# Optimization experiments

Measured on AMD Instinct MI355X. Metric: run time of the kernel, lower is better.

Reference implementation:

```python
import jax, jax.numpy as jnp
import numpy as np

N, E, W, H, NXF, NDF = 131072, 8, 128, 64, 10, 4
DX = 3 + 3 * 2 * NXF  # 63
DV = 3 + 3 * 2 * NDF  # 27
TEMP = 0.166667


def pe(x, degree):
    # positional encoding: [x, sin(2^i x), cos(2^i x)]
    y = jnp.concatenate([(2.0 ** i) * x for i in range(degree)], -1)
    return jnp.concatenate([x, jnp.sin(y), jnp.cos(y)], -1)


def setup_inputs() -> dict:
    key = jax.random.key(0)
    ks = jax.random.split(key, 8)
    s = 0.05
    return {
        'x': jax.random.normal(ks[0], (N, 6), jnp.float32),
        'W_enc': jax.random.normal(ks[1], (DX, W), jnp.float32) * s,
        'b_enc': jnp.zeros((W,), jnp.float32),
        'W_sh': jax.random.normal(ks[2], (E, W, W), jnp.float32) * s,
        'b_sh': jnp.zeros((E, W), jnp.float32),
        'w_sig': jax.random.normal(ks[3], (W,), jnp.float32) * s,
        'b_sig': jnp.zeros((1,), jnp.float32),
        'W_r1': jax.random.normal(ks[4], (E, W + DV, H), jnp.float32) * s,
        'b_r1': jnp.zeros((E, H), jnp.float32),
        'W_r2': jax.random.normal(ks[5], (E, H, 3), jnp.float32) * s,
        'b_r2': jnp.zeros((E, 3), jnp.float32),
    }


def reference(x, W_enc, b_enc, W_sh, b_sh, w_sig, b_sig, W_r1, b_r1, W_r2, b_r2):
    xyz = pe(x[:, :3], NXF)          # [N, 63]
    vd = pe(x[:, 3:6], NDF)          # [N, 27]
    y = jax.nn.relu(xyz @ W_enc + b_enc)  # encoding_xyz -> [N, W]
    # all shape experts at once: [N, E, W]
    shape_out = jax.nn.relu(jnp.einsum('nd,edh->neh', y, W_sh) + b_sh)
    # shared sigma head, softplus keeps sigma > 0: [N, E]
    sigmas = jax.nn.softplus(jnp.einsum('neh,h->ne', shape_out, w_sig) + b_sig)
    log_logits = jax.nn.log_softmax(jnp.log(sigmas + 1e-10) / TEMP, axis=-1)
    # gumbel-softmax (tau=1, torch default) with fixed noise key
    u = jax.random.uniform(jax.random.key(42), sigmas.shape, jnp.float32)
    g = -jnp.log(-jnp.log(u + 1e-20) + 1e-20)
    gates_soft = jax.nn.softmax(log_logits + g, axis=-1)
    index = jnp.argmax(gates_soft, axis=-1)  # [N]
    hard = jax.nn.one_hot(index, E, dtype=sigmas.dtype)
    # straight-through hard gates
    gates_hard = hard - jax.lax.stop_gradient(gates_soft) + gates_soft
    sigmas_pooled = jnp.take_along_axis(sigmas, index[:, None], axis=-1)  # [N, 1]
    # rgb experts: concat(shape_out_i, viewdir) -> MLP -> sigmoid rgb, gated sum
    vdb = jnp.broadcast_to(vd[:, None, :], (vd.shape[0], E, DV))
    inp = jnp.concatenate([shape_out, vdb], axis=-1)  # [N, E, W+27]
    h = jax.nn.relu(jnp.einsum('nec,ech->neh', inp, W_r1) + b_r1)
    rgb = jax.nn.sigmoid(jnp.einsum('neh,eho->neo', h, W_r2) + b_r2)  # [N, E, 3]
    rgbs = jnp.sum(rgb * gates_hard[:, :, None], axis=1)  # [N, 3]
    return jnp.concatenate([rgbs, sigmas_pooled], axis=-1)  # [N, 4]
```

## Files before the change

### kernel.cpp

```cpp
#include <hip/hip_runtime.h>
#include <hip/hip_bf16.h>


#define NPTS 131072
#define PT 64
#define NTH 256
#define NBLK (NPTS / PT)
#define INV2048 (1.0f / 2048.0f)

#define WS_ENC_H 0
#define WS_ENC_L 8192
#define WS_SH_H  16384
#define WS_SH_L  147456
#define WS_R1_H  278528

#define OFF_YH   0
#define OFF_B    17408
#define OFF_RED  38912
#define SMEM_SZ  40960

#define S_LIST(s) (*(int*)(smem + OFF_B + (s) * 336 + 320))
#define S_BID(p)  (*(int*)(smem + OFF_B + (p) * 336 + 324))
#define S_CNT(e)  (*(int*)(smem + OFF_B + (e) * 336 + 328))
#define S_OFF(e)  (*(int*)(smem + OFF_B + (e) * 336 + 332))

typedef __attribute__((ext_vector_type(8))) _Float16 f16x8;
typedef __attribute__((ext_vector_type(4))) _Float16 f16x4;
typedef __attribute__((ext_vector_type(4))) float f32x4;

#define MFMA(a, b, c) __builtin_amdgcn_mfma_f32_16x16x32_f16((a), (b), (c), 0, 0, 0)

__device__ __forceinline__ unsigned rotl32(unsigned x, int d) {
  return (x << d) | (x >> (32 - d));
}

__device__ __forceinline__ float gumbel_for(unsigned flat) {
  const unsigned k0 = 0u, k1 = 42u;
  const unsigned ks2 = k0 ^ k1 ^ 0x1BD11BDAu;
  unsigned x0 = 0u + k0;
  unsigned x1 = flat + k1;
#define TF_RND(r) { x0 += x1; x1 = rotl32(x1, r); x1 ^= x0; }
  TF_RND(13) TF_RND(15) TF_RND(26) TF_RND(6)
  x0 += k1;  x1 += ks2 + 1u;
  TF_RND(17) TF_RND(29) TF_RND(16) TF_RND(24)
  x0 += ks2; x1 += k0 + 2u;
  TF_RND(13) TF_RND(15) TF_RND(26) TF_RND(6)
  x0 += k0;  x1 += k1 + 3u;
  TF_RND(17) TF_RND(29) TF_RND(16) TF_RND(24)
  x0 += k1;  x1 += ks2 + 4u;
  TF_RND(13) TF_RND(15) TF_RND(26) TF_RND(6)
  x0 += ks2; x1 += k0 + 5u;
#undef TF_RND
  unsigned bits = x0 ^ x1;
  float u = __uint_as_float((bits >> 9) | 0x3f800000u) - 1.0f;
  return -logf(-logf(u + 1e-20f) + 1e-20f);
}

__global__ void prep_kernel(const float* __restrict__ W_enc,
                            const float* __restrict__ W_sh,
                            const float* __restrict__ W_r1,
                            _Float16* __restrict__ ws) {
  int idx = blockIdx.x * 256 + threadIdx.x;
  if (idx < 8192) {
    int tile = idx >> 9, r = idx & 511;
    int L = r >> 3, j = r & 7;
    int nt = tile >> 1, kt = tile & 1;
    int k = kt * 32 + (L >> 4) * 8 + j;
    int n = nt * 16 + (L & 15);
    float v = (k < 63) ? W_enc[k * 128 + n] : 0.0f;
    _Float16 h = (_Float16)v;
    ws[WS_ENC_H + idx] = h;
    ws[WS_ENC_L + idx] = (_Float16)((v - (float)h) * 2048.0f);
  } else if (idx < 8192 + 131072) {
    int s = idx - 8192;
    int tile = s >> 9, r = s & 511;
    int L = r >> 3, j = r & 7;
    int e = tile >> 5, nt = (tile >> 2) & 7, kt = tile & 3;
    int k = kt * 32 + (L >> 4) * 8 + j;
    int n = nt * 16 + (L & 15);
    float v = W_sh[e * 16384 + k * 128 + n];
    _Float16 h = (_Float16)v;
    ws[WS_SH_H + s] = h;
    ws[WS_SH_L + s] = (_Float16)((v - (float)h) * 2048.0f);
  } else if (idx < 8192 + 131072 + 81920) {
    int s = idx - (8192 + 131072);
    int tile = s >> 9, r = s & 511;
    int L = r >> 3, j = r & 7;
    int e = tile / 20, rr = tile % 20;
    int nt = rr / 5, kt = rr % 5;
    int k = kt * 32 + (L >> 4) * 8 + j;
    int n = nt * 16 + (L & 15);
    float v = (k < 155) ? W_r1[e * 9920 + k * 64 + n] : 0.0f;
    ws[WS_R1_H + s] = (_Float16)v;
  }
}

__global__ __launch_bounds__(NTH, 3)
void nerf_moe_kernel(const float* __restrict__ x,
                     const float* __restrict__ b_enc,
                     const float* __restrict__ b_sh,
                     const float* __restrict__ w_sig, const float* __restrict__ b_sig,
                     const float* __restrict__ b_r1,
                     const float* __restrict__ W_r2,  const float* __restrict__ b_r2,
                     const _Float16* __restrict__ wsw,
                     float* __restrict__ out) {
  __shared__ __align__(16) unsigned char smem[SMEM_SZ];
  _Float16* sYh  = (_Float16*)(smem + OFF_YH);
  float*    sH   = (float*)(smem + OFF_YH);
  _Float16* sYl  = (_Float16*)(smem + OFF_B);
  _Float16* sPEh = (_Float16*)(smem + OFF_B);
  _Float16* sPEl = (_Float16*)(smem + OFF_B + 9216);
  _Float16* sSB  = (_Float16*)(smem + OFF_B);
  float*    sRed = (float*)(smem + OFF_RED);

  const int t  = threadIdx.x;
  const int w  = t >> 6;
  const int L  = t & 63;
  const int q  = L >> 4;
  const int c  = L & 15;
  const int n0 = blockIdx.x * PT;

  sRed[t] = 0.0f;
  sRed[t + 256] = 0.0f;

  for (int idx = t; idx < PT * 64; idx += NTH) {
    int p = idx >> 6, f = idx & 63;
    const float* xr = x + (size_t)(n0 + p) * 6;
    float v;
    if (f < 3)       v = xr[f];
    else if (f < 33) { int g = f - 3;  v = sinf(xr[g % 3] * (float)(1 << (g / 3))); }
    else if (f < 63) { int g = f - 33; v = cosf(xr[g % 3] * (float)(1 << (g / 3))); }
    else             v = 0.0f;
    _Float16 h = (_Float16)v;
    sPEh[p * 72 + f] = h;
    sPEl[p * 72 + f] = (_Float16)((v - (float)h) * 2048.0f);
  }
  __syncthreads();

  {
    f16x8 beh[2][2], bel[2][2];
    #pragma unroll
    for (int ntL = 0; ntL < 2; ++ntL)
      #pragma unroll
      for (int kt = 0; kt < 2; ++kt) {
        int tile = (2 * w + ntL) * 2 + kt;
        beh[ntL][kt] = *(const f16x8*)(wsw + WS_ENC_H + tile * 512 + L * 8);
        bel[ntL][kt] = *(const f16x8*)(wsw + WS_ENC_L + tile * 512 + L * 8);
      }
    f32x4 a1[4][2], a2[4][2];
    #pragma unroll
    for (int mt = 0; mt < 4; ++mt)
      #pragma unroll
      for (int ntL = 0; ntL < 2; ++ntL) { a1[mt][ntL] = (f32x4)0.0f; a2[mt][ntL] = (f32x4)0.0f; }
    #pragma unroll
    for (int half = 0; half < 2; ++half) {
      f16x8 pah[2][2], pal[2][2];
      #pragma unroll
      for (int m = 0; m < 2; ++m)
        #pragma unroll
        for (int kt = 0; kt < 2; ++kt) {
          int off = ((half * 2 + m) * 16 + c) * 72 + kt * 32 + q * 8;
          pah[m][kt] = *(const f16x8*)(sPEh + off);
          pal[m][kt] = *(const f16x8*)(sPEl + off);
        }
      #pragma unroll
      for (int kt = 0; kt < 2; ++kt)
        #pragma unroll
        for (int m = 0; m < 2; ++m)
          #pragma unroll
          for (int ntL = 0; ntL < 2; ++ntL) {
            int mt = half * 2 + m;
            a1[mt][ntL] = MFMA(pah[m][kt], beh[ntL][kt], a1[mt][ntL]);
            a2[mt][ntL] = MFMA(pah[m][kt], bel[ntL][kt], a2[mt][ntL]);
            a2[mt][ntL] = MFMA(pal[m][kt], beh[ntL][kt], a2[mt][ntL]);
          }
      asm volatile("" ::: "memory");
    }
    __syncthreads();
    float bb0 = b_enc[(2 * w) * 16 + c];
    float bb1 = b_enc[(2 * w + 1) * 16 + c];
    #pragma unroll
    for (int mt = 0; mt < 4; ++mt)
      #pragma unroll
      for (int ntL = 0; ntL < 2; ++ntL) {
        float bb = ntL ? bb1 : bb0;
        int col = (2 * w + ntL) * 16 + c;
        #pragma unroll
        for (int r = 0; r < 4; ++r) {
          float v = fmaxf(a1[mt][ntL][r] + a2[mt][ntL][r] * INV2048 + bb, 0.0f);
          int row = mt * 16 + q * 4 + r;
          _Float16 h = (_Float16)v;
          sYh[row * 136 + col] = h;
          sYl[row * 136 + col] = (_Float16)((v - (float)h) * 2048.0f);
        }
      }
  }
  __syncthreads();

  f16x8 Ah[4][3];
  #pragma unroll
  for (int nt = 0; nt < 4; ++nt)
    #pragma unroll
    for (int kt = 0; kt < 3; ++kt)
      Ah[nt][kt] = *(const f16x8*)(sYh + (nt * 16 + c) * 136 + kt * 32 + q * 8);
  const f32x4 wsv0 = *(const f32x4*)(w_sig + (2 * w) * 16 + q * 4);
  const f32x4 wsv1 = *(const f32x4*)(w_sig + (2 * w + 1) * 16 + q * 4);

  float psum[4] = {0.f, 0.f, 0.f, 0.f};

  #pragma unroll 1
  for (int s = 0; s < 16; ++s) {
    int e = s >> 1, i = s & 1;
    int tbase = (e * 8 + 2 * w + i) * 4;
    f16x8 bh[4], bl[4];
    #pragma unroll
    for (int kt = 0; kt < 4; ++kt) {
      bh[kt] = *(const f16x8*)(wsw + WS_SH_H + (tbase + kt) * 512 + L * 8);
      bl[kt] = *(const f16x8*)(wsw + WS_SH_L + (tbase + kt) * 512 + L * 8);
    }
    f32x4 bb = *(const f32x4*)(b_sh + e * 128 + (2 * w + i) * 16 + q * 4);

    f32x4 a1[4], a2[4];
    #pragma unroll
    for (int nt = 0; nt < 4; ++nt) { a1[nt] = (f32x4)0.0f; a2[nt] = (f32x4)0.0f; }
    #pragma unroll
    for (int kt = 0; kt < 4; ++kt)
      #pragma unroll
      for (int nt = 0; nt < 4; ++nt) {
        f16x8 al = *(const f16x8*)(sYl + (nt * 16 + c) * 136 + kt * 32 + q * 8);
        f16x8 ah;
        if (kt < 3) ah = Ah[nt][kt];
        else        ah = *(const f16x8*)(sYh + (nt * 16 + c) * 136 + kt * 32 + q * 8);
        a1[nt] = MFMA(bh[kt], ah, a1[nt]);
        a2[nt] = MFMA(bl[kt], ah, a2[nt]);
        a2[nt] = MFMA(bh[kt], al, a2[nt]);
      }
    f32x4 wv = (s & 1) ? wsv1 : wsv0;
    #pragma unroll
    for (int nt = 0; nt < 4; ++nt)
      #pragma unroll
      for (int r = 0; r < 4; ++r) {
        float sv = fmaxf(fmaf(a2[nt][r], INV2048, a1[nt][r]) + bb[r], 0.0f);
        psum[nt] = fmaf(sv, wv[r], psum[nt]);
      }
    if (s & 1) {
      #pragma unroll
      for (int nt = 0; nt < 4; ++nt) {
        float v = psum[nt];
        v += __shfl_xor(v, 16);
        v += __shfl_xor(v, 32);
        if (q == 0) atomicAdd(sRed + e * 64 + nt * 16 + c, v);
        psum[nt] = 0.f;
      }
    }
  }
  __syncthreads();

  {
    int pt = t >> 2;
    int eb = (t & 3) * 2;
    float best = -1e30f, bsig = 0.0f;
    int bide = 0;
    const float bs = b_sig[0];
    #pragma unroll
    for (int j = 0; j < 2; ++j) {
      int e = eb + j;
      float s = sRed[e * 64 + pt];
      float dotv = s + bs;
      float sig = fmaxf(dotv, 0.0f) + log1pf(expf(-fabsf(dotv)));
      float z = logf(sig + 1e-10f) / 0.166667f;
      float score = z + gumbel_for((unsigned)((n0 + pt) * 8 + e));
      if (score > best) { best = score; bsig = sig; bide = e; }
    }
    #pragma unroll
    for (int m = 1; m <= 2; m <<= 1) {
      float oS  = __shfl_xor(best, m);
      float oSg = __shfl_xor(bsig, m);
      int   oI  = __shfl_xor(bide, m);
      if (oS > best || (oS == best && oI < bide)) { best = oS; bsig = oSg; bide = oI; }
    }
    if ((t & 3) == 0) {
      S_BID(pt) = bide;
      out[(size_t)(n0 + pt) * 4 + 3] = bsig;
    }
  }
  __syncthreads();

  if (t < 8) {
    int cnt = 0;
    for (int p = 0; p < PT; ++p) cnt += (S_BID(p) == t);
    S_CNT(t) = cnt;
  }
  __syncthreads();
  if (t < 8) {
    int off = 0;
    for (int i = 0; i < t; ++i) off += S_CNT(i);
    S_OFF(t) = off;
    int k = off;
    for (int p = 0; p < PT; ++p) if (S_BID(p) == t) { S_LIST(k) = p; k++; }
  }
  __syncthreads();

  for (int idx = t; idx < PT * 32; idx += NTH) {
    int s = idx >> 5, cc = idx & 31;
    int pt = S_LIST(s);
    const float* xr = x + (size_t)(n0 + pt) * 6 + 3;
    float v;
    if (cc < 3)       v = xr[cc];
    else if (cc < 15) { int g = cc - 3;  v = sinf(xr[g % 3] * (float)(1 << (g / 3))); }
    else if (cc < 27) { int g = cc - 15; v = cosf(xr[g % 3] * (float)(1 << (g / 3))); }
    else              v = 0.0f;
    sSB[s * 168 + 128 + cc] = (_Float16)v;
  }
  #pragma unroll 1
  for (int ei = 0; ei < 2; ++ei) {
    int e = 2 * w + ei;
    int cnt = S_CNT(e), off = S_OFF(e);
    for (int base = 0; base < cnt; base += 16) {
      int sidx = base + c; if (sidx >= cnt) sidx = cnt - 1;
      int pt = S_LIST(off + sidx);
      f16x8 yb[4];
      #pragma unroll
      for (int kt = 0; kt < 4; ++kt)
        yb[kt] = *(const f16x8*)(sYh + pt * 136 + kt * 32 + q * 8);
      f32x4 acc[8];
      #pragma unroll
      for (int jt = 0; jt < 8; ++jt) acc[jt] = (f32x4)0.0f;
      #pragma unroll
      for (int jt = 0; jt < 8; ++jt)
        #pragma unroll
        for (int kt = 0; kt < 4; ++kt) {
          f16x8 a = *(const f16x8*)(wsw + WS_SH_H + ((e * 8 + jt) * 4 + kt) * 512 + L * 8);
          acc[jt] = MFMA(a, yb[kt], acc[jt]);
        }
      bool wr = (base + c) < cnt;
      int slot = off + base + c;
      #pragma unroll
      for (int jt = 0; jt < 8; ++jt) {
        f32x4 bb = *(const f32x4*)(b_sh + e * 128 + jt * 16 + q * 4);
        f16x4 v;
        #pragma unroll
        for (int r = 0; r < 4; ++r)
          v[r] = (_Float16)fmaxf(acc[jt][r] + bb[r], 0.0f);
        if (wr) *(f16x4*)(sSB + slot * 168 + jt * 16 + q * 4) = v;
      }
    }
  }
  __syncthreads();

  #pragma unroll 1
  for (int ei = 0; ei < 2; ++ei) {
    int e = 2 * w + ei;
    int cnt = S_CNT(e), off = S_OFF(e);
    for (int base = 0; base < cnt; base += 16) {
      int sidx = base + c; if (sidx >= cnt) sidx = cnt - 1;
      int slot = off + sidx;
      f16x8 ag[5];
      #pragma unroll
      for (int kt = 0; kt < 5; ++kt)
        ag[kt] = *(const f16x8*)(sSB + slot * 168 + kt * 32 + q * 8);
      f32x4 hacc[4];
      #pragma unroll
      for (int nt = 0; nt < 4; ++nt) hacc[nt] = (f32x4)0.0f;
      #pragma unroll
      for (int nt = 0; nt < 4; ++nt)
        #pragma unroll
        for (int kt = 0; kt < 5; ++kt) {
          f16x8 bf = *(const f16x8*)(wsw + WS_R1_H + ((e * 4 + nt) * 5 + kt) * 512 + L * 8);
          hacc[nt] = MFMA(ag[kt], bf, hacc[nt]);
        }
      #pragma unroll
      for (int nt = 0; nt < 4; ++nt) {
        float bb = b_r1[e * 64 + nt * 16 + c];
        #pragma unroll
        for (int r = 0; r < 4; ++r) {
          int m = q * 4 + r;
          if (base + m < cnt)
            sH[(off + base + m) * 68 + nt * 16 + c] = fmaxf(hacc[nt][r] + bb, 0.0f);
        }
      }
    }
  }
  __syncthreads();

  if (t < 192) {
    int s = t / 3, o = t - s * 3;
    int pt = S_LIST(s);
    int e = S_BID(pt);
    float a = b_r2[e * 3 + o];
    const float* w2 = W_r2 + e * 192 + o;
    #pragma unroll
    for (int jj = 0; jj < 64; jj += 4) {
      f32x4 h4 = *(const f32x4*)(sH + s * 68 + jj);
      a = fmaf(h4.x, w2[jj * 3], a);
      a = fmaf(h4.y, w2[jj * 3 + 3], a);
      a = fmaf(h4.z, w2[jj * 3 + 6], a);
      a = fmaf(h4.w, w2[jj * 3 + 9], a);
    }
    out[(size_t)(n0 + pt) * 4 + o] = 1.0f / (1.0f + expf(-a));
  }
}

extern "C" void kernel_launch(void* const* d_in, const int* in_sizes, int n_in,
                              void* d_out, int out_size, void* d_ws, size_t ws_size,
                              hipStream_t stream) {
  (void)in_sizes; (void)n_in; (void)ws_size; (void)out_size;
  const float* x     = (const float*)d_in[0];
  const float* W_enc = (const float*)d_in[1];
  const float* b_enc = (const float*)d_in[2];
  const float* W_sh  = (const float*)d_in[3];
  const float* b_sh  = (const float*)d_in[4];
  const float* w_sig = (const float*)d_in[5];
  const float* b_sig = (const float*)d_in[6];
  const float* W_r1  = (const float*)d_in[7];
  const float* b_r1  = (const float*)d_in[8];
  const float* W_r2  = (const float*)d_in[9];
  const float* b_r2  = (const float*)d_in[10];
  _Float16* ws = (_Float16*)d_ws;
  float* outp = (float*)d_out;
  prep_kernel<<<864, 256, 0, stream>>>(W_enc, W_sh, W_r1, ws);
  nerf_moe_kernel<<<NBLK, NTH, 0, stream>>>(x, b_enc, b_sh, w_sig, b_sig,
                                            b_r1, W_r2, b_r2, ws, outp);
}
```

Before: 298.8 us.

## Raise wave priority around MFMA clusters and build expert lists with ballot

Wraps each MFMA cluster in the encoder, shape-expert, routed shape and rgb-layer GEMMs with s_setprio(1)/s_setprio(0). The aim is to let waves that are issuing matrix ops get scheduling priority while other waves do loads, so compute and memory overlap better. It also replaces the serial per-expert counting and list building, done by 8 threads looping over 64 points, with a single-wave ballot/popcount scan, which removes one barrier and the serial loops. The added compiler barriers and priority toggles may limit instruction scheduling freedom.

```diff
diff --git a/kernel.cpp b/kernel.cpp
--- a/kernel.cpp
+++ b/kernel.cpp
@@ -163,6 +163,7 @@
           pah[m][kt] = *(const f16x8*)(sPEh + off);
           pal[m][kt] = *(const f16x8*)(sPEl + off);
         }
+      __builtin_amdgcn_s_setprio(1);
       #pragma unroll
       for (int kt = 0; kt < 2; ++kt)
         #pragma unroll
@@ -174,6 +175,7 @@
             a2[mt][ntL] = MFMA(pah[m][kt], bel[ntL][kt], a2[mt][ntL]);
             a2[mt][ntL] = MFMA(pal[m][kt], beh[ntL][kt], a2[mt][ntL]);
           }
+      __builtin_amdgcn_s_setprio(0);
       asm volatile("" ::: "memory");
     }
     __syncthreads();
@@ -223,6 +225,7 @@
     f32x4 a1[4], a2[4];
     #pragma unroll
     for (int nt = 0; nt < 4; ++nt) { a1[nt] = (f32x4)0.0f; a2[nt] = (f32x4)0.0f; }
+    __builtin_amdgcn_s_setprio(1);
     #pragma unroll
     for (int kt = 0; kt < 4; ++kt)
       #pragma unroll
@@ -235,6 +238,7 @@
         a2[nt] = MFMA(bl[kt], ah, a2[nt]);
         a2[nt] = MFMA(bh[kt], al, a2[nt]);
       }
+    __builtin_amdgcn_s_setprio(0);
     f32x4 wv = (s & 1) ? wsv1 : wsv0;
     #pragma unroll
     for (int nt = 0; nt < 4; ++nt)
@@ -286,18 +290,21 @@
   }
   __syncthreads();
 
-  if (t < 8) {
-    int cnt = 0;
-    for (int p = 0; p < PT; ++p) cnt += (S_BID(p) == t);
-    S_CNT(t) = cnt;
-  }
-  __syncthreads();
-  if (t < 8) {
+  if (t < 64) {
+    int bid = S_BID(t);
+    unsigned long long below = t ? ((~0ULL) >> (64 - t)) : 0ULL;
     int off = 0;
-    for (int i = 0; i < t; ++i) off += S_CNT(i);
-    S_OFF(t) = off;
-    int k = off;
-    for (int p = 0; p < PT; ++p) if (S_BID(p) == t) { S_LIST(k) = p; k++; }
+    #pragma unroll
+    for (int e = 0; e < 8; ++e) {
+      unsigned long long m = __ballot(bid == e);
+      int cnt = __popcll(m);
+      if (t == e) { S_CNT(e) = cnt; S_OFF(e) = off; }
+      if (bid == e) {
+        int rank = __popcll(m & below);
+        S_LIST(off + rank) = t;
+      }
+      off += cnt;
+    }
   }
   __syncthreads();
 
@@ -327,12 +334,20 @@
       #pragma unroll
       for (int jt = 0; jt < 8; ++jt) acc[jt] = (f32x4)0.0f;
       #pragma unroll
-      for (int jt = 0; jt < 8; ++jt)
-        #pragma unroll
-        for (int kt = 0; kt < 4; ++kt) {
-          f16x8 a = *(const f16x8*)(wsw + WS_SH_H + ((e * 8 + jt) * 4 + kt) * 512 + L * 8);
-          acc[jt] = MFMA(a, yb[kt], acc[jt]);
+      for (int jh = 0; jh < 2; ++jh) {
+        __builtin_amdgcn_s_setprio(1);
+        #pragma unroll
+        for (int jt2 = 0; jt2 < 4; ++jt2) {
+          int jt = jh * 4 + jt2;
+          #pragma unroll
+          for (int kt = 0; kt < 4; ++kt) {
+            f16x8 a = *(const f16x8*)(wsw + WS_SH_H + ((e * 8 + jt) * 4 + kt) * 512 + L * 8);
+            acc[jt] = MFMA(a, yb[kt], acc[jt]);
+          }
         }
+        __builtin_amdgcn_s_setprio(0);
+        asm volatile("" ::: "memory");
+      }
       bool wr = (base + c) < cnt;
       int slot = off + base + c;
       #pragma unroll
@@ -363,12 +378,20 @@
       #pragma unroll
       for (int nt = 0; nt < 4; ++nt) hacc[nt] = (f32x4)0.0f;
       #pragma unroll
-      for (int nt = 0; nt < 4; ++nt)
-        #pragma unroll
-        for (int kt = 0; kt < 5; ++kt) {
-          f16x8 bf = *(const f16x8*)(wsw + WS_R1_H + ((e * 4 + nt) * 5 + kt) * 512 + L * 8);
-          hacc[nt] = MFMA(ag[kt], bf, hacc[nt]);
+      for (int nh = 0; nh < 2; ++nh) {
+        __builtin_amdgcn_s_setprio(1);
+        #pragma unroll
+        for (int nt2 = 0; nt2 < 2; ++nt2) {
+          int nt = nh * 2 + nt2;
+          #pragma unroll
+          for (int kt = 0; kt < 5; ++kt) {
+            f16x8 bf = *(const f16x8*)(wsw + WS_R1_H + ((e * 4 + nt) * 5 + kt) * 512 + L * 8);
+            hacc[nt] = MFMA(ag[kt], bf, hacc[nt]);
+          }
         }
+        __builtin_amdgcn_s_setprio(0);
+        asm volatile("" ::: "memory");
+      }
       #pragma unroll
       for (int nt = 0; nt < 4; ++nt) {
         float bb = b_r1[e * 64 + nt * 16 + c];
```

Measured after the change: 256.1 us. 14.3% less time.
